# Kernel tuning notes

Measured on AMD Instinct MI355X. Metric: run time of the kernel, lower is better.

The kernel has to match this reference:

```python
import jax, jax.numpy as jnp
import numpy as np

B, N, D, H, DK, DV, R = 4, 256, 256, 8, 32, 32, 64
EPS = 1e-6


def setup_inputs() -> dict:
    key = jax.random.key(0)
    ks = jax.random.split(key, 16)
    s = D ** -0.5
    return {
        "q": jax.random.normal(ks[0], (B, N, D), jnp.float32),
        "k": jax.random.normal(ks[1], (B, N, D), jnp.float32),
        "v": jax.random.normal(ks[2], (B, N, D), jnp.float32),
        "mask": jax.random.randint(ks[3], (B, N, N), 0, 2).astype(jnp.int32),
        "link": jax.random.uniform(ks[4], (B, N, N, R), jnp.float32),
        "Wq": jax.random.normal(ks[5], (D, H * DK), jnp.float32) * s,
        "Wk": jax.random.normal(ks[6], (D, H * DK), jnp.float32) * s,
        "Wr": jax.random.normal(ks[7], (D, H * DK), jnp.float32) * s,
        "Wv": jax.random.normal(ks[8], (D, H * DV), jnp.float32) * s,
        "Wvv": jax.random.normal(ks[9], (D, H * DV), jnp.float32) * s,
        "relationE": jax.random.normal(ks[10], (R, D), jnp.float32) * s,
        "Wo": jax.random.normal(ks[11], (H * DV, D), jnp.float32) * s,
        "gamma": jnp.ones((D,), jnp.float32),
        "beta": jnp.zeros((D,), jnp.float32),
    }


def reference(q, k, v, mask, link, Wq, Wk, Wr, Wv, Wvv, relationE, Wo, gamma, beta):
    # rela_num != 0 branch of Ruleformer MultiHeadAttention (dropout = identity, eval mode).
    residual = q
    b, n, d = q.shape
    # per-head projections of X (== q == residual in this branch): [b,h,n,dk]
    Xq = (q @ Wq).reshape(b, n, H, DK).transpose(0, 2, 1, 3)
    Xk = (q @ Wk).reshape(b, n, H, DK).transpose(0, 2, 1, 3)
    Xv = (q @ Wv).reshape(b, n, H, DV).transpose(0, 2, 1, 3)

    # calcE: relation-biased scores. Rk[b,i,j,h,d] = (link @ relationE @ Wr)
    Rk = jnp.einsum('bijr,re->bije', link, relationE @ Wr).reshape(b, n, n, H, DK)
    # attn[b,h,i,j] = Xq[b,h,i] . (Xk[b,h,j] + Rk[b,i,j,h])
    attn = jnp.einsum('bhid,bhjd->bhij', Xq, Xk)
    attn = attn + jnp.einsum('bijhd,bhid->bhij', Rk, Xq)
    attn = attn / (DK ** 0.5)
    attn = jnp.where(mask[:, None, :, :] == 0, -1e9, attn)
    alpha = jax.nn.softmax(attn, axis=-1)  # [b,h,n,n]

    # calcZ: Z[b,h,i] = sum_j alpha[b,h,i,j] * (Xv[b,h,j] + Rv[b,i,j,h])
    Rv = jnp.einsum('bijr,re->bije', link, relationE @ Wvv).reshape(b, n, n, H, DV)
    Z = jnp.einsum('bhij,bhjd->bhid', alpha, Xv)
    Z = Z + jnp.einsum('bhij,bijhd->bhid', alpha, Rv)

    out = Z.transpose(0, 2, 1, 3).reshape(b, n, H * DV) @ Wo
    out = out + residual
    mu = out.mean(-1, keepdims=True)
    var = ((out - mu) ** 2).mean(-1, keepdims=True)
    out = (out - mu) * jax.lax.rsqrt(var + EPS) * gamma + beta
    return out, alpha
```

## Files before the change

### kernel.cpp

```cpp
#include <hip/hip_runtime.h>
#include <math.h>

constexpr int B_ = 4, N_ = 256, D_ = 256, H_ = 8, DK_ = 32, DV_ = 32, R_ = 64;
constexpr float SCALE_ = 0.17677669529663687f;
constexpr float EPS_ = 1e-6f;

__global__ __launch_bounds__(256) void projekev_kernel(
        const float* __restrict__ q, const float* __restrict__ Wq,
        const float* __restrict__ Wk, const float* __restrict__ Wv,
        const float* __restrict__ relE, const float* __restrict__ Wr,
        const float* __restrict__ Wvv, float* __restrict__ Xq,
        float* __restrict__ Xk, float* __restrict__ Xv,
        float* __restrict__ Ek, float* __restrict__ Ev) {
    int blk = blockIdx.x;
    int t = threadIdx.x;
    __shared__ __align__(16) float ash[32 * 65];
    __shared__ __align__(16) float bsh[32 * 64];
    const float *src, *W;
    int rowbase, cbase, ct;
    float* dstE = nullptr;
    if (blk < 192) {
        ct = blk >> 4;
        int rt = blk & 15;
        src = q; rowbase = rt * 64;
        if (ct < 4)      { W = Wq; cbase = ct * 64; }
        else if (ct < 8) { W = Wk; cbase = (ct - 4) * 64; }
        else             { W = Wv; cbase = (ct - 8) * 64; }
    } else {
        int e = blk - 192;
        src = relE; rowbase = 0; ct = -1;
        W = (e < 4) ? Wr : Wvv;
        dstE = (e < 4) ? Ek : Ev;
        cbase = (e & 3) * 64;
    }
    int ti = t >> 4, tj = t & 15;
    float acc[4][4] = {{0.f}};
    for (int kc = 0; kc < 8; ++kc) {
        __syncthreads();
#pragma unroll
        for (int kk = 0; kk < 2; ++kk) {
            int m = t + kk * 256;
            int i = m >> 3, kq = m & 7;
            float4 v = *(const float4*)(src + (size_t)(rowbase + i) * 256 + kc * 32 + kq * 4);
            ash[(kq * 4 + 0) * 65 + i] = v.x;
            ash[(kq * 4 + 1) * 65 + i] = v.y;
            ash[(kq * 4 + 2) * 65 + i] = v.z;
            ash[(kq * 4 + 3) * 65 + i] = v.w;
        }
#pragma unroll
        for (int kk = 0; kk < 2; ++kk) {
            int m = t + kk * 256;
            int k = m >> 4, j4 = m & 15;
            float4 v = *(const float4*)(W + (size_t)(kc * 32 + k) * 256 + cbase + j4 * 4);
            *(float4*)(bsh + k * 64 + j4 * 4) = v;
        }
        __syncthreads();
#pragma unroll 8
        for (int k = 0; k < 32; ++k) {
            float4 av = *(const float4*)(ash + k * 65 + ti * 4);
            float4 bv = *(const float4*)(bsh + k * 64 + tj * 4);
            acc[0][0] += av.x * bv.x; acc[0][1] += av.x * bv.y;
            acc[0][2] += av.x * bv.z; acc[0][3] += av.x * bv.w;
            acc[1][0] += av.y * bv.x; acc[1][1] += av.y * bv.y;
            acc[1][2] += av.y * bv.z; acc[1][3] += av.y * bv.w;
            acc[2][0] += av.z * bv.x; acc[2][1] += av.z * bv.y;
            acc[2][2] += av.z * bv.z; acc[2][3] += av.z * bv.w;
            acc[3][0] += av.w * bv.x; acc[3][1] += av.w * bv.y;
            acc[3][2] += av.w * bv.z; acc[3][3] += av.w * bv.w;
        }
    }
    if (dstE) {
#pragma unroll
        for (int a = 0; a < 4; ++a) {
            int row = ti * 4 + a;
            *(float4*)(dstE + (size_t)row * 256 + cbase + tj * 4) =
                make_float4(acc[a][0], acc[a][1], acc[a][2], acc[a][3]);
        }
    } else {
        float* dst = (ct < 4) ? Xq : (ct < 8) ? Xk : Xv;
        int gcol = (ct & 3) * 64 + tj * 4;
        int h = gcol >> 5, dk = gcol & 31;
#pragma unroll
        for (int a = 0; a < 4; ++a) {
            int row = rowbase + ti * 4 + a;
            int bb = row >> 8, n = row & 255;
            *(float4*)(dst + ((size_t)(bb * 8 + h) * 256 + n) * 32 + dk) =
                make_float4(acc[a][0], acc[a][1], acc[a][2], acc[a][3]);
        }
    }
}

__global__ __launch_bounds__(256) void qkT_kernel(
        const float* __restrict__ Xq, const float* __restrict__ Xk,
        const float* __restrict__ Ek, float* __restrict__ qk,
        float* __restrict__ T) {
    int x = blockIdx.x;
    int jt = x & 3, it = (x >> 2) & 3, bh = x >> 4;
    int b = bh >> 3, h = bh & 7;
    int t = threadIdx.x;
    __shared__ __align__(16) float xqsh[32 * 64];
    __shared__ __align__(16) float xksh[32 * 64];
    __shared__ __align__(16) float eksh[32 * 64];
#pragma unroll
    for (int k = 0; k < 2; ++k) {
        int m = t + k * 256;
        int i = m >> 3, dq4 = m & 7;
        float4 v = *(const float4*)(Xq + ((size_t)(bh * 256 + it * 64 + i)) * 32 + dq4 * 4);
        xqsh[(dq4 * 4 + 0) * 64 + i] = v.x;
        xqsh[(dq4 * 4 + 1) * 64 + i] = v.y;
        xqsh[(dq4 * 4 + 2) * 64 + i] = v.z;
        xqsh[(dq4 * 4 + 3) * 64 + i] = v.w;
        float4 u = *(const float4*)(Xk + ((size_t)(bh * 256 + jt * 64 + i)) * 32 + dq4 * 4);
        xksh[(dq4 * 4 + 0) * 64 + i] = u.x;
        xksh[(dq4 * 4 + 1) * 64 + i] = u.y;
        xksh[(dq4 * 4 + 2) * 64 + i] = u.z;
        xksh[(dq4 * 4 + 3) * 64 + i] = u.w;
    }
    if (jt == 0) {
        int r = t >> 2, dq = t & 3;
#pragma unroll
        for (int kk = 0; kk < 2; ++kk) {
            int dq4 = dq + kk * 4;
            float4 v = *(const float4*)(Ek + r * 256 + h * 32 + dq4 * 4);
            eksh[(dq4 * 4 + 0) * 64 + r] = v.x;
            eksh[(dq4 * 4 + 1) * 64 + r] = v.y;
            eksh[(dq4 * 4 + 2) * 64 + r] = v.z;
            eksh[(dq4 * 4 + 3) * 64 + r] = v.w;
        }
    }
    __syncthreads();
    int ti = t >> 4, tj = t & 15;
    float acc[4][4] = {{0.f}};
#pragma unroll 8
    for (int dk = 0; dk < 32; ++dk) {
        float4 av = *(const float4*)(xqsh + dk * 64 + ti * 4);
        float4 bv = *(const float4*)(xksh + dk * 64 + tj * 4);
        acc[0][0] += av.x * bv.x; acc[0][1] += av.x * bv.y;
        acc[0][2] += av.x * bv.z; acc[0][3] += av.x * bv.w;
        acc[1][0] += av.y * bv.x; acc[1][1] += av.y * bv.y;
        acc[1][2] += av.y * bv.z; acc[1][3] += av.y * bv.w;
        acc[2][0] += av.z * bv.x; acc[2][1] += av.z * bv.y;
        acc[2][2] += av.z * bv.z; acc[2][3] += av.z * bv.w;
        acc[3][0] += av.w * bv.x; acc[3][1] += av.w * bv.y;
        acc[3][2] += av.w * bv.z; acc[3][3] += av.w * bv.w;
    }
#pragma unroll
    for (int a = 0; a < 4; ++a) {
        int i = it * 64 + ti * 4 + a;
        *(float4*)(qk + ((size_t)(bh * 256 + i)) * 256 + jt * 64 + tj * 4) =
            make_float4(acc[a][0], acc[a][1], acc[a][2], acc[a][3]);
    }
    if (jt == 0) {
        float tacc[4][4] = {{0.f}};
#pragma unroll 8
        for (int dk = 0; dk < 32; ++dk) {
            float4 av = *(const float4*)(xqsh + dk * 64 + ti * 4);
            float4 ev = *(const float4*)(eksh + dk * 64 + tj * 4);
            tacc[0][0] += av.x * ev.x; tacc[0][1] += av.x * ev.y;
            tacc[0][2] += av.x * ev.z; tacc[0][3] += av.x * ev.w;
            tacc[1][0] += av.y * ev.x; tacc[1][1] += av.y * ev.y;
            tacc[1][2] += av.y * ev.z; tacc[1][3] += av.y * ev.w;
            tacc[2][0] += av.z * ev.x; tacc[2][1] += av.z * ev.y;
            tacc[2][2] += av.z * ev.z; tacc[2][3] += av.z * ev.w;
            tacc[3][0] += av.w * ev.x; tacc[3][1] += av.w * ev.y;
            tacc[3][2] += av.w * ev.z; tacc[3][3] += av.w * ev.w;
        }
#pragma unroll
        for (int a = 0; a < 4; ++a) {
            int i = it * 64 + ti * 4 + a;
            *(float4*)(T + ((size_t)(b * 256 + i)) * 512 + h * 64 + tj * 4) =
                make_float4(tacc[a][0], tacc[a][1], tacc[a][2], tacc[a][3]);
        }
    }
}

__global__ __launch_bounds__(256) void expsz_kernel(
        const float* __restrict__ link, const float* __restrict__ Tg,
        const float* __restrict__ qk, const int* __restrict__ mask,
        const float* __restrict__ Xv, float* __restrict__ alphaU,
        float* __restrict__ Spart, float* __restrict__ Zpart) {
    int v = ((blockIdx.x & 7) << 9) | (blockIdx.x >> 3);
    int bi = v >> 2, jc = v & 3;
    int b = bi >> 8, i = bi & 255;
    int t = threadIdx.x;
    int g = t >> 6, jl = t & 63;
    int j0 = jc * 64;
    int h0 = g * 2, h1 = g * 2 + 1;

    __shared__ __align__(16) float linksh[64 * 68];
    __shared__ __align__(16) float Tsh[8 * 68];
    __shared__ __align__(16) float expsh[8 * 66];
    __shared__ __align__(16) float4 zsh[4 * 64];

    {
        const float4* lp4 = (const float4*)(link + ((size_t)bi * 256 + j0) * 64);
#pragma unroll
        for (int k = 0; k < 4; ++k) {
            int m = t + k * 256;
            int j = m >> 4, rq = m & 15;
            *(float4*)(linksh + j * 68 + rq * 4) = lp4[m];
        }
    }
    for (int m = t; m < 512; m += 256)
        Tsh[(m >> 6) * 68 + (m & 63)] = Tg[(size_t)bi * 512 + m];
    float qv0 = qk[((size_t)(b * 8 + h0) * 256 + i) * 256 + j0 + jl];
    float qv1 = qk[((size_t)(b * 8 + h1) * 256 + i) * 256 + j0 + jl];
    int mv = mask[((size_t)(b * 256 + i)) * 256 + j0 + jl];
    __syncthreads();

    float s0 = 0.f, s1 = 0.f;
    {
        const float4* lr = (const float4*)(linksh + jl * 68);
        const float4* t0 = (const float4*)(Tsh + h0 * 68);
        const float4* t1 = (const float4*)(Tsh + h1 * 68);
#pragma unroll
        for (int rq = 0; rq < 16; ++rq) {
            float4 lv = lr[rq];
            float4 a0 = t0[rq], a1 = t1[rq];
            s0 += lv.x * a0.x + lv.y * a0.y + lv.z * a0.z + lv.w * a0.w;
            s1 += lv.x * a1.x + lv.y * a1.y + lv.z * a1.z + lv.w * a1.w;
        }
    }
    s0 = (qv0 + s0) * SCALE_;
    s1 = (qv1 + s1) * SCALE_;
    if (mv == 0) { s0 = -1e9f; s1 = -1e9f; }
    float e0 = __expf(s0), e1 = __expf(s1);
    expsh[h0 * 66 + jl] = e0;
    expsh[h1 * 66 + jl] = e1;
    alphaU[((size_t)(b * 8 + h0) * 256 + i) * 256 + j0 + jl] = e0;
    alphaU[((size_t)(b * 8 + h1) * 256 + i) * 256 + j0 + jl] = e1;
    __syncthreads();

    {
        float acc0 = 0.f, acc1 = 0.f;
        const float* ls = linksh + jl;
        const float* e0p = expsh + h0 * 66;
        const float* e1p = expsh + h1 * 66;
#pragma unroll 8
        for (int j = 0; j < 64; ++j) {
            float lv = ls[j * 68];
            acc0 += e0p[j] * lv;
            acc1 += e1p[j] * lv;
        }
        float* sp = Spart + ((size_t)bi * 4 + jc) * 512;
        sp[h0 * 64 + jl] = acc0;
        sp[h1 * 64 + jl] = acc1;
    }

    {
        int o = jl;
        int h = o >> 3, dv4 = o & 7;
        const float4* xv4 = (const float4*)Xv +
            (((size_t)(b * 8 + h)) * 256 + j0 + g * 16) * 8 + dv4;
        const float* ep = expsh + h * 66 + g * 16;
        float4 z = make_float4(0.f, 0.f, 0.f, 0.f);
#pragma unroll
        for (int j = 0; j < 16; ++j) {
            float a = ep[j];
            float4 x = xv4[j * 8];
            z.x += a * x.x; z.y += a * x.y; z.z += a * x.z; z.w += a * x.w;
        }
        zsh[g * 64 + o] = z;
    }
    __syncthreads();
    if (t < 64) {
        float4 z0 = zsh[t], z1 = zsh[64 + t], z2 = zsh[128 + t], z3 = zsh[192 + t];
        float4 z = make_float4(z0.x + z1.x + z2.x + z3.x,
                               z0.y + z1.y + z2.y + z3.y,
                               z0.z + z1.z + z2.z + z3.z,
                               z0.w + z1.w + z2.w + z3.w);
        *(float4*)(Zpart + ((size_t)bi * 4 + jc) * 256 + t * 4) = z;
    }
}

__global__ __launch_bounds__(256) void finz_kernel(
        const float* __restrict__ Spart, const float* __restrict__ Zpart,
        const float* __restrict__ Ev, float* __restrict__ alpha,
        float* __restrict__ Z) {
    int bi = blockIdx.x;
    int b = bi >> 8, i = bi & 255;
    int t = threadIdx.x;
    int lane = t & 63, g = t >> 6;
    __shared__ __align__(16) float Ssh[8 * 68];
    __shared__ float invsh[8];
    __shared__ float redsh[32];

    for (int m = t; m < 512; m += 256) {
        float sv = Spart[((size_t)bi * 4 + 0) * 512 + m] +
                   Spart[((size_t)bi * 4 + 1) * 512 + m] +
                   Spart[((size_t)bi * 4 + 2) * 512 + m] +
                   Spart[((size_t)bi * 4 + 3) * 512 + m];
        Ssh[(m >> 6) * 68 + (m & 63)] = sv;
    }
    float a[8];
#pragma unroll
    for (int k = 0; k < 8; ++k)
        a[k] = alpha[((size_t)(b * 8 + k) * 256 + i) * 256 + t];
    float zq = Zpart[((size_t)bi * 4 + 0) * 256 + t] +
               Zpart[((size_t)bi * 4 + 1) * 256 + t] +
               Zpart[((size_t)bi * 4 + 2) * 256 + t] +
               Zpart[((size_t)bi * 4 + 3) * 256 + t];
#pragma unroll
    for (int k = 0; k < 8; ++k) {
        float v = a[k];
        for (int off = 32; off > 0; off >>= 1) v += __shfl_xor(v, off);
        if (lane == 0) redsh[k * 4 + g] = v;
    }
    __syncthreads();
    if (t < 8)
        invsh[t] = 1.f / (redsh[t * 4] + redsh[t * 4 + 1] +
                          redsh[t * 4 + 2] + redsh[t * 4 + 3]);
    __syncthreads();
#pragma unroll
    for (int k = 0; k < 8; ++k)
        alpha[((size_t)(b * 8 + k) * 256 + i) * 256 + t] = a[k] * invsh[k];
    {
        int h = t >> 5, dv = t & 31;
        float acc = 0.f;
        const float* sp = Ssh + h * 68;
        const float* evp = Ev + h * 32 + dv;
#pragma unroll 4
        for (int r = 0; r < 64; ++r) acc += sp[r] * evp[r * 256];
        Z[(size_t)bi * 256 + t] = (zq + acc) * invsh[h];
    }
}

__global__ __launch_bounds__(256) void out_kernel(
        const float* __restrict__ Z, const float* __restrict__ Wo,
        const float* __restrict__ q, const float* __restrict__ gamma,
        const float* __restrict__ beta, float* __restrict__ out) {
    int row0 = blockIdx.x * 2;
    int t = threadIdx.x;
    __shared__ __align__(16) float zsh[512];
    __shared__ float redsh[16];
    zsh[t] = Z[(size_t)row0 * 256 + t];
    zsh[256 + t] = Z[(size_t)row0 * 256 + 256 + t];
    __syncthreads();
    float a0 = q[(size_t)row0 * 256 + t];
    float a1 = q[(size_t)(row0 + 1) * 256 + t];
    for (int d4 = 0; d4 < 64; ++d4) {
        float w0 = Wo[(d4 * 4 + 0) * 256 + t];
        float w1 = Wo[(d4 * 4 + 1) * 256 + t];
        float w2 = Wo[(d4 * 4 + 2) * 256 + t];
        float w3 = Wo[(d4 * 4 + 3) * 256 + t];
        float4 z0v = *(const float4*)(zsh + d4 * 4);
        float4 z1v = *(const float4*)(zsh + 256 + d4 * 4);
        a0 += z0v.x * w0 + z0v.y * w1 + z0v.z * w2 + z0v.w * w3;
        a1 += z1v.x * w0 + z1v.y * w1 + z1v.z * w2 + z1v.w * w3;
    }
    int lane = t & 63, wv = t >> 6;
    float acc2[2] = {a0, a1};
#pragma unroll
    for (int rr = 0; rr < 2; ++rr) {
        float v = acc2[rr], v2 = acc2[rr] * acc2[rr];
        for (int off = 32; off > 0; off >>= 1) {
            v += __shfl_xor(v, off);
            v2 += __shfl_xor(v2, off);
        }
        if (lane == 0) {
            redsh[rr * 8 + wv] = v;
            redsh[rr * 8 + 4 + wv] = v2;
        }
    }
    __syncthreads();
#pragma unroll
    for (int rr = 0; rr < 2; ++rr) {
        float sum = redsh[rr * 8 + 0] + redsh[rr * 8 + 1] + redsh[rr * 8 + 2] + redsh[rr * 8 + 3];
        float sum2 = redsh[rr * 8 + 4] + redsh[rr * 8 + 5] + redsh[rr * 8 + 6] + redsh[rr * 8 + 7];
        float mu = sum * (1.f / 256.f);
        float var = sum2 * (1.f / 256.f) - mu * mu;
        float dev = acc2[rr] - mu;
        out[(size_t)(row0 + rr) * 256 + t] = dev * rsqrtf(var + EPS_) * gamma[t] + beta[t];
    }
}

extern "C" void kernel_launch(void* const* d_in, const int* in_sizes, int n_in,
                              void* d_out, int out_size, void* d_ws, size_t ws_size,
                              hipStream_t stream) {
    const float* q     = (const float*)d_in[0];
    const int*   mask  = (const int*)d_in[3];
    const float* link  = (const float*)d_in[4];
    const float* Wq    = (const float*)d_in[5];
    const float* Wk    = (const float*)d_in[6];
    const float* Wr    = (const float*)d_in[7];
    const float* Wv    = (const float*)d_in[8];
    const float* Wvv   = (const float*)d_in[9];
    const float* relE  = (const float*)d_in[10];
    const float* Wo    = (const float*)d_in[11];
    const float* gamma = (const float*)d_in[12];
    const float* beta  = (const float*)d_in[13];

    float* out   = (float*)d_out;
    float* alpha = out + B_ * N_ * D_;

    float* ws = (float*)d_ws;
    float* Ek    = ws;
    float* Ev    = Ek + 16384;
    float* Xq    = Ev + 16384;
    float* Xk    = Xq + 262144;
    float* Xv    = Xk + 262144;
    float* T     = Xv + 262144;
    float* qkbuf = T + 524288;
    float* Spart = qkbuf + 2097152;
    float* Zpart = Spart + 2097152;

    projekev_kernel<<<200, 256, 0, stream>>>(q, Wq, Wk, Wv, relE, Wr, Wvv,
                                             Xq, Xk, Xv, Ek, Ev);
    qkT_kernel<<<512, 256, 0, stream>>>(Xq, Xk, Ek, qkbuf, T);
    expsz_kernel<<<4096, 256, 0, stream>>>(link, T, qkbuf, mask, Xv,
                                           alpha, Spart, Zpart);
    finz_kernel<<<1024, 256, 0, stream>>>(Spart, Zpart, Ev, alpha, Xq);
    out_kernel<<<512, 256, 0, stream>>>(Xq, Wo, q, gamma, beta, out);
}
```

Before: 186.5 us.

## Fuse softmax finalize into output kernel and split T blocks in qkT

Merges the finz and out kernels into one finout kernel that handles two rows per block. It normalizes alpha using per-chunk exp sums that expsz now produces with wave reductions, so alpha no longer has to be re-read just to compute row sums. The qkT kernel moves the T computation into separate extra blocks instead of doing it inside the jt==0 blocks, which removes that load imbalance and frees shared memory. In exchange there is one more small partial-sum buffer, and the fused kernel runs only 512 blocks with a serial loop over its two rows.

Result: no change. 183.7 us (-1.5%).

```diff
diff --git a/kernel.cpp b/kernel.cpp
--- a/kernel.cpp
+++ b/kernel.cpp
@@ -95,12 +95,14 @@
         const float* __restrict__ Ek, float* __restrict__ qk,
         float* __restrict__ T) {
     int x = blockIdx.x;
-    int jt = x & 3, it = (x >> 2) & 3, bh = x >> 4;
-    int b = bh >> 3, h = bh & 7;
     int t = threadIdx.x;
     __shared__ __align__(16) float xqsh[32 * 64];
-    __shared__ __align__(16) float xksh[32 * 64];
-    __shared__ __align__(16) float eksh[32 * 64];
+    __shared__ __align__(16) float bsh2[32 * 64];
+    bool isT = (x >= 512);
+    int jt, it, bh;
+    if (!isT) { jt = x & 3; it = (x >> 2) & 3; bh = x >> 4; }
+    else      { int e = x - 512; jt = 0; it = e & 3; bh = e >> 2; }
+    int b = bh >> 3, h = bh & 7;
 #pragma unroll
     for (int k = 0; k < 2; ++k) {
         int m = t + k * 256;
@@ -110,22 +112,28 @@
         xqsh[(dq4 * 4 + 1) * 64 + i] = v.y;
         xqsh[(dq4 * 4 + 2) * 64 + i] = v.z;
         xqsh[(dq4 * 4 + 3) * 64 + i] = v.w;
-        float4 u = *(const float4*)(Xk + ((size_t)(bh * 256 + jt * 64 + i)) * 32 + dq4 * 4);
-        xksh[(dq4 * 4 + 0) * 64 + i] = u.x;
-        xksh[(dq4 * 4 + 1) * 64 + i] = u.y;
-        xksh[(dq4 * 4 + 2) * 64 + i] = u.z;
-        xksh[(dq4 * 4 + 3) * 64 + i] = u.w;
-    }
-    if (jt == 0) {
+    }
+    if (!isT) {
+#pragma unroll
+        for (int k = 0; k < 2; ++k) {
+            int m = t + k * 256;
+            int i = m >> 3, dq4 = m & 7;
+            float4 u = *(const float4*)(Xk + ((size_t)(bh * 256 + jt * 64 + i)) * 32 + dq4 * 4);
+            bsh2[(dq4 * 4 + 0) * 64 + i] = u.x;
+            bsh2[(dq4 * 4 + 1) * 64 + i] = u.y;
+            bsh2[(dq4 * 4 + 2) * 64 + i] = u.z;
+            bsh2[(dq4 * 4 + 3) * 64 + i] = u.w;
+        }
+    } else {
         int r = t >> 2, dq = t & 3;
 #pragma unroll
         for (int kk = 0; kk < 2; ++kk) {
             int dq4 = dq + kk * 4;
             float4 v = *(const float4*)(Ek + r * 256 + h * 32 + dq4 * 4);
-            eksh[(dq4 * 4 + 0) * 64 + r] = v.x;
-            eksh[(dq4 * 4 + 1) * 64 + r] = v.y;
-            eksh[(dq4 * 4 + 2) * 64 + r] = v.z;
-            eksh[(dq4 * 4 + 3) * 64 + r] = v.w;
+            bsh2[(dq4 * 4 + 0) * 64 + r] = v.x;
+            bsh2[(dq4 * 4 + 1) * 64 + r] = v.y;
+            bsh2[(dq4 * 4 + 2) * 64 + r] = v.z;
+            bsh2[(dq4 * 4 + 3) * 64 + r] = v.w;
         }
     }
     __syncthreads();
@@ -134,7 +142,7 @@
 #pragma unroll 8
     for (int dk = 0; dk < 32; ++dk) {
         float4 av = *(const float4*)(xqsh + dk * 64 + ti * 4);
-        float4 bv = *(const float4*)(xksh + dk * 64 + tj * 4);
+        float4 bv = *(const float4*)(bsh2 + dk * 64 + tj * 4);
         acc[0][0] += av.x * bv.x; acc[0][1] += av.x * bv.y;
         acc[0][2] += av.x * bv.z; acc[0][3] += av.x * bv.w;
         acc[1][0] += av.y * bv.x; acc[1][1] += av.y * bv.y;
@@ -144,32 +152,19 @@
         acc[3][0] += av.w * bv.x; acc[3][1] += av.w * bv.y;
         acc[3][2] += av.w * bv.z; acc[3][3] += av.w * bv.w;
     }
-#pragma unroll
-    for (int a = 0; a < 4; ++a) {
-        int i = it * 64 + ti * 4 + a;
-        *(float4*)(qk + ((size_t)(bh * 256 + i)) * 256 + jt * 64 + tj * 4) =
-            make_float4(acc[a][0], acc[a][1], acc[a][2], acc[a][3]);
-    }
-    if (jt == 0) {
-        float tacc[4][4] = {{0.f}};
-#pragma unroll 8
-        for (int dk = 0; dk < 32; ++dk) {
-            float4 av = *(const float4*)(xqsh + dk * 64 + ti * 4);
-            float4 ev = *(const float4*)(eksh + dk * 64 + tj * 4);
-            tacc[0][0] += av.x * ev.x; tacc[0][1] += av.x * ev.y;
-            tacc[0][2] += av.x * ev.z; tacc[0][3] += av.x * ev.w;
-            tacc[1][0] += av.y * ev.x; tacc[1][1] += av.y * ev.y;
-            tacc[1][2] += av.y * ev.z; tacc[1][3] += av.y * ev.w;
-            tacc[2][0] += av.z * ev.x; tacc[2][1] += av.z * ev.y;
-            tacc[2][2] += av.z * ev.z; tacc[2][3] += av.z * ev.w;
-            tacc[3][0] += av.w * ev.x; tacc[3][1] += av.w * ev.y;
-            tacc[3][2] += av.w * ev.z; tacc[3][3] += av.w * ev.w;
-        }
+    if (!isT) {
+#pragma unroll
+        for (int a = 0; a < 4; ++a) {
+            int i = it * 64 + ti * 4 + a;
+            *(float4*)(qk + ((size_t)(bh * 256 + i)) * 256 + jt * 64 + tj * 4) =
+                make_float4(acc[a][0], acc[a][1], acc[a][2], acc[a][3]);
+        }
+    } else {
 #pragma unroll
         for (int a = 0; a < 4; ++a) {
             int i = it * 64 + ti * 4 + a;
             *(float4*)(T + ((size_t)(b * 256 + i)) * 512 + h * 64 + tj * 4) =
-                make_float4(tacc[a][0], tacc[a][1], tacc[a][2], tacc[a][3]);
+                make_float4(acc[a][0], acc[a][1], acc[a][2], acc[a][3]);
         }
     }
 }
@@ -178,7 +173,8 @@
         const float* __restrict__ link, const float* __restrict__ Tg,
         const float* __restrict__ qk, const int* __restrict__ mask,
         const float* __restrict__ Xv, float* __restrict__ alphaU,
-        float* __restrict__ Spart, float* __restrict__ Zpart) {
+        float* __restrict__ Spart, float* __restrict__ Zpart,
+        float* __restrict__ esumP) {
     int v = ((blockIdx.x & 7) << 9) | (blockIdx.x >> 3);
     int bi = v >> 2, jc = v & 3;
     int b = bi >> 8, i = bi & 255;
@@ -229,6 +225,17 @@
     expsh[h1 * 66 + jl] = e1;
     alphaU[((size_t)(b * 8 + h0) * 256 + i) * 256 + j0 + jl] = e0;
     alphaU[((size_t)(b * 8 + h1) * 256 + i) * 256 + j0 + jl] = e1;
+    {
+        float v0 = e0, v1 = e1;
+        for (int off = 32; off > 0; off >>= 1) {
+            v0 += __shfl_xor(v0, off);
+            v1 += __shfl_xor(v1, off);
+        }
+        if (jl == 0) {
+            esumP[((size_t)bi * 4 + jc) * 8 + h0] = v0;
+            esumP[((size_t)bi * 4 + jc) * 8 + h1] = v1;
+        }
+    }
     __syncthreads();
 
     {
@@ -273,69 +280,61 @@
     }
 }
 
-__global__ __launch_bounds__(256) void finz_kernel(
+__global__ __launch_bounds__(256) void finout_kernel(
         const float* __restrict__ Spart, const float* __restrict__ Zpart,
-        const float* __restrict__ Ev, float* __restrict__ alpha,
-        float* __restrict__ Z) {
-    int bi = blockIdx.x;
-    int b = bi >> 8, i = bi & 255;
+        const float* __restrict__ esumP, const float* __restrict__ Ev,
+        const float* __restrict__ Wo, const float* __restrict__ q,
+        const float* __restrict__ gamma, const float* __restrict__ beta,
+        float* __restrict__ alpha, float* __restrict__ out) {
+    int row0 = blockIdx.x * 2;
+    int b = row0 >> 8;
     int t = threadIdx.x;
-    int lane = t & 63, g = t >> 6;
+    int lane = t & 63, wv = t >> 6;
     __shared__ __align__(16) float Ssh[8 * 68];
-    __shared__ float invsh[8];
-    __shared__ float redsh[32];
-
-    for (int m = t; m < 512; m += 256) {
-        float sv = Spart[((size_t)bi * 4 + 0) * 512 + m] +
-                   Spart[((size_t)bi * 4 + 1) * 512 + m] +
-                   Spart[((size_t)bi * 4 + 2) * 512 + m] +
-                   Spart[((size_t)bi * 4 + 3) * 512 + m];
-        Ssh[(m >> 6) * 68 + (m & 63)] = sv;
-    }
-    float a[8];
-#pragma unroll
-    for (int k = 0; k < 8; ++k)
-        a[k] = alpha[((size_t)(b * 8 + k) * 256 + i) * 256 + t];
-    float zq = Zpart[((size_t)bi * 4 + 0) * 256 + t] +
-               Zpart[((size_t)bi * 4 + 1) * 256 + t] +
-               Zpart[((size_t)bi * 4 + 2) * 256 + t] +
-               Zpart[((size_t)bi * 4 + 3) * 256 + t];
-#pragma unroll
-    for (int k = 0; k < 8; ++k) {
-        float v = a[k];
-        for (int off = 32; off > 0; off >>= 1) v += __shfl_xor(v, off);
-        if (lane == 0) redsh[k * 4 + g] = v;
-    }
-    __syncthreads();
-    if (t < 8)
-        invsh[t] = 1.f / (redsh[t * 4] + redsh[t * 4 + 1] +
-                          redsh[t * 4 + 2] + redsh[t * 4 + 3]);
-    __syncthreads();
-#pragma unroll
-    for (int k = 0; k < 8; ++k)
-        alpha[((size_t)(b * 8 + k) * 256 + i) * 256 + t] = a[k] * invsh[k];
-    {
-        int h = t >> 5, dv = t & 31;
-        float acc = 0.f;
-        const float* sp = Ssh + h * 68;
-        const float* evp = Ev + h * 32 + dv;
+    __shared__ __align__(16) float zsh[512];
+    __shared__ float invsh[16];
+    __shared__ float redsh[16];
+
+    for (int rr = 0; rr < 2; ++rr) {
+        int row = row0 + rr;
+        int i = row & 255;
+        __syncthreads();
+        if (t < 8) {
+            float es = esumP[((size_t)row * 4 + 0) * 8 + t] +
+                       esumP[((size_t)row * 4 + 1) * 8 + t] +
+                       esumP[((size_t)row * 4 + 2) * 8 + t] +
+                       esumP[((size_t)row * 4 + 3) * 8 + t];
+            invsh[rr * 8 + t] = 1.f / es;
+        }
+        for (int m = t; m < 512; m += 256) {
+            float sv = Spart[((size_t)row * 4 + 0) * 512 + m] +
+                       Spart[((size_t)row * 4 + 1) * 512 + m] +
+                       Spart[((size_t)row * 4 + 2) * 512 + m] +
+                       Spart[((size_t)row * 4 + 3) * 512 + m];
+            Ssh[(m >> 6) * 68 + (m & 63)] = sv;
+        }
+        __syncthreads();
+#pragma unroll
+        for (int k = 0; k < 8; ++k) {
+            size_t off = ((size_t)(b * 8 + k) * 256 + i) * 256 + t;
+            alpha[off] *= invsh[rr * 8 + k];
+        }
+        {
+            int h = t >> 5, dv = t & 31;
+            float zq = Zpart[((size_t)row * 4 + 0) * 256 + t] +
+                       Zpart[((size_t)row * 4 + 1) * 256 + t] +
+                       Zpart[((size_t)row * 4 + 2) * 256 + t] +
+                       Zpart[((size_t)row * 4 + 3) * 256 + t];
+            float acc = 0.f;
+            const float* sp = Ssh + h * 68;
+            const float* evp = Ev + h * 32 + dv;
 #pragma unroll 4
-        for (int r = 0; r < 64; ++r) acc += sp[r] * evp[r * 256];
-        Z[(size_t)bi * 256 + t] = (zq + acc) * invsh[h];
-    }
-}
-
-__global__ __launch_bounds__(256) void out_kernel(
-        const float* __restrict__ Z, const float* __restrict__ Wo,
-        const float* __restrict__ q, const float* __restrict__ gamma,
-        const float* __restrict__ beta, float* __restrict__ out) {
-    int row0 = blockIdx.x * 2;
-    int t = threadIdx.x;
-    __shared__ __align__(16) float zsh[512];
-    __shared__ float redsh[16];
-    zsh[t] = Z[(size_t)row0 * 256 + t];
-    zsh[256 + t] = Z[(size_t)row0 * 256 + 256 + t];
-    __syncthreads();
+            for (int r = 0; r < 64; ++r) acc += sp[r] * evp[r * 256];
+            zsh[rr * 256 + t] = (zq + acc) * invsh[rr * 8 + h];
+        }
+    }
+    __syncthreads();
+
     float a0 = q[(size_t)row0 * 256 + t];
     float a1 = q[(size_t)(row0 + 1) * 256 + t];
     for (int d4 = 0; d4 < 64; ++d4) {
@@ -348,7 +347,6 @@
         a0 += z0v.x * w0 + z0v.y * w1 + z0v.z * w2 + z0v.w * w3;
         a1 += z1v.x * w0 + z1v.y * w1 + z1v.z * w2 + z1v.w * w3;
     }
-    int lane = t & 63, wv = t >> 6;
     float acc2[2] = {a0, a1};
 #pragma unroll
     for (int rr = 0; rr < 2; ++rr) {
@@ -403,12 +401,13 @@
     float* qkbuf = T + 524288;
     float* Spart = qkbuf + 2097152;
     float* Zpart = Spart + 2097152;
+    float* esumP = Zpart + 1048576;
 
     projekev_kernel<<<200, 256, 0, stream>>>(q, Wq, Wk, Wv, relE, Wr, Wvv,
                                              Xq, Xk, Xv, Ek, Ev);
-    qkT_kernel<<<512, 256, 0, stream>>>(Xq, Xk, Ek, qkbuf, T);
+    qkT_kernel<<<640, 256, 0, stream>>>(Xq, Xk, Ek, qkbuf, T);
     expsz_kernel<<<4096, 256, 0, stream>>>(link, T, qkbuf, mask, Xv,
-                                           alpha, Spart, Zpart);
-    finz_kernel<<<1024, 256, 0, stream>>>(Spart, Zpart, Ev, alpha, Xq);
-    out_kernel<<<512, 256, 0, stream>>>(Xq, Wo, q, gamma, beta, out);
+                                           alpha, Spart, Zpart, esumP);
+    finout_kernel<<<512, 256, 0, stream>>>(Spart, Zpart, esumP, Ev, Wo, q,
+                                           gamma, beta, alpha, out);
 }
```
